# Kernel tuning notes

Hardware: AMD Instinct MI355X
Metric: run time of the kernel (lower is better)

## Reference

```python
import jax, jax.numpy as jnp
import numpy as np
from jax.scipy.linalg import expm

B, Q, F, R, T, H = 2048, 16, 512, 400, 50, 256
STEPS = 100
DT = 1.0 / STEPS
COH = 50.0  # coherence_time


def setup_inputs() -> dict:
    ks = jax.random.split(jax.random.key(0), 48)
    it = iter(range(48))
    def rn(shape, s=1.0):
        return jax.random.normal(ks[next(it)], shape, dtype=jnp.float32) * s
    A = rn((Q, Q)); Bm = rn((Q, Q))
    d = {
        'molecular_features': rn((B, F)),
        'noise': rn((B, T, R), 0.1),          # torch.randn_like * 0.1
        'amp_re': rn((B, Q)), 'amp_im': rn((B, Q)),
        'H_re': (A + A.T) / 2.0,               # hermitized: real part symmetric
        'H_im': (Bm - Bm.T) / 2.0,             # imag part antisymmetric
        'gpc': rn((R,)),
        'bw1': rn((256, Q + F), (Q + F) ** -0.5), 'bb1': rn((256,), 0.01),
        'bw2': rn((128, 256), 256 ** -0.5), 'bb2': rn((128,), 0.01),
        'bw3': rn((R, 128), 128 ** -0.5), 'bb3': rn((R,), 0.01),
    }
    ins = [R, H, H]
    for l in range(3):
        d[f'Wih{l}'] = rn((4 * H, ins[l]), ins[l] ** -0.5)
        d[f'Whh{l}'] = rn((4 * H, H), H ** -0.5)
        d[f'bih{l}'] = rn((4 * H,), 0.01)
        d[f'bhh{l}'] = rn((4 * H,), 0.01)
    d.update({
        'cw1': rn((512, H + R), (H + R) ** -0.5), 'cb1': rn((512,), 0.01),
        'cw2': rn((256, 512), 512 ** -0.5), 'cb2': rn((256,), 0.01),
        'cw3': rn((64, 256), 256 ** -0.5), 'cb3': rn((64,), 0.01),
        'cw4': rn((1, 64), 64 ** -0.5), 'cb4': rn((1,), 0.01),
    })
    return d


def _lstm_layer(x, Wih, Whh, bih, bhh):
    # PyTorch LSTM gate order: i, f, g, o
    def step(carry, xt):
        h, c = carry
        z = xt @ Wih.T + h @ Whh.T + bih + bhh
        ig, fg, gg, og = jnp.split(z, 4, axis=-1)
        c = jax.nn.sigmoid(fg) * c + jax.nn.sigmoid(ig) * jnp.tanh(gg)
        h = jax.nn.sigmoid(og) * jnp.tanh(c)
        return (h, c), h
    n = x.shape[0]
    init = (jnp.zeros((n, H), x.dtype), jnp.zeros((n, H), x.dtype))
    (hT, _), hs = jax.lax.scan(step, init, jnp.swapaxes(x, 0, 1))
    return jnp.swapaxes(hs, 0, 1), hT


def _forward(molecular_features, noise, amp_re, amp_im, H_re, H_im, gpc,
             bw1, bb1, bw2, bb2, bw3, bb3,
             Wih0, Whh0, bih0, bhh0, Wih1, Whh1, bih1, bhh1, Wih2, Whh2, bih2, bhh2,
             cw1, cb1, cw2, cb2, cw3, cb3, cw4, cb4):
    Hp = (H_re + 1j * H_im).astype(jnp.complex64)
    amp = (amp_re + 1j * amp_im).astype(jnp.complex64)
    amp = amp / jnp.linalg.norm(amp, axis=-1, keepdims=True)  # F.normalize
    # molecular interaction Hamiltonian (real part only, as in source)
    M = jnp.einsum('bi,ij->bij', molecular_features[:, :Q], H_re)
    def qstep(a, step):
        t = step * DT
        Ht = Hp[None, :, :] + M * t                 # [B,Q,Q] complex
        U = jax.vmap(expm)(-1j * Ht * DT)           # per-sample matrix_exp
        a = jnp.einsum('bij,bj->bi', U, a) * jnp.exp(-t / COH)
        return a, None
    amp, _ = jax.lax.scan(qstep, amp, jnp.arange(STEPS, dtype=jnp.float32))
    obs = (jnp.abs(amp) ** 2).astype(jnp.float32)   # quantum observables
    bio = jnp.concatenate([obs, molecular_features], axis=-1)  # [B, Q+F]
    h1 = jax.nn.relu(bio @ bw1.T + bb1)
    h2 = jnp.tanh(h1 @ bw2.T + bb2)
    receptor = jax.nn.sigmoid(h2 @ bw3.T + bb3)     # [B, R]
    # biological signal transduction
    g_amp = receptor * jax.nn.sigmoid(gpc)
    adapt = jnp.exp(-jnp.arange(T, dtype=jnp.float32) / 10.0)[None, :, None]
    seq = g_amp[:, None, :] * adapt + noise         # [B, T, R]
    x, hT = _lstm_layer(seq, Wih0, Whh0, bih0, bhh0)
    x, hT = _lstm_layer(x, Wih1, Whh1, bih1, bhh1)
    x, hT = _lstm_layer(x, Wih2, Whh2, bih2, bhh2)  # hT: last-layer hidden [B,H]
    cf = jnp.concatenate([hT, receptor], axis=-1)   # [B, H+R]
    c1 = jax.nn.relu(cf @ cw1.T + cb1)
    c2 = jax.nn.relu(c1 @ cw2.T + cb2)
    c3 = jnp.tanh(c2 @ cw3.T + cb3)
    cons = jnp.mean(jax.nn.sigmoid(c3 @ cw4.T + cb4))
    valence = jnp.mean(jnp.tanh(x), axis=(1, 2))    # [B]
    return receptor, x, valence, cons, amp


def reference(molecular_features, noise, amp_re, amp_im, H_re, H_im, gpc,
              bw1, bb1, bw2, bb2, bw3, bb3,
              Wih0, Whh0, bih0, bhh0, Wih1, Whh1, bih1, bhh1, Wih2, Whh2, bih2, bhh2,
              cw1, cb1, cw2, cb2, cw3, cb3, cw4, cb4):
    receptor, seq, valence, cons, amp = _forward(
        molecular_features, noise, amp_re, amp_im, H_re, H_im, gpc,
        bw1, bb1, bw2, bb2, bw3, bb3,
        Wih0, Whh0, bih0, bhh0, Wih1, Whh1, bih1, bhh1, Wih2, Whh2, bih2, bhh2,
        cw1, cb1, cw2, cb2, cw3, cb3, cw4, cb4)
    # von Neumann entanglement entropy across a 2/2 qubit bipartition (Q=16 -> 4x4)
    half = 2 ** ((int(np.log2(Q))) // 2)
    rs = amp.reshape(amp.shape[0], half, -1)
    rho = jnp.einsum('bij,bik->bjk', rs, jnp.conj(rs))
    ev = jnp.clip(jnp.linalg.eigvals(rho).real, 1e-12, None)
    ent = jnp.mean(-jnp.sum(ev * jnp.log(ev), axis=-1))
    return receptor, seq, valence, cons, ent
```

## Files before the change

### kernel.cpp

```cpp
#include <hip/hip_runtime.h>
#include <stdint.h>


using short8 = __attribute__((ext_vector_type(8))) short;
using f32x4  = __attribute__((ext_vector_type(4))) float;

#define DEV static __device__ __forceinline__

typedef const __attribute__((address_space(1))) void GV;
typedef __attribute__((address_space(3))) void LV;
DEV void gload16(const void* g, void* l) {
  __builtin_amdgcn_global_load_lds((GV*)g, (LV*)l, 16, 0, 0);
}

DEV ushort f2b(float x) {
  union { float f; uint32_t u; } v; v.f = x;
  uint32_t r = v.u + 0x7FFFu + ((v.u >> 16) & 1u);
  return (ushort)(r >> 16);
}
DEV float b2f(ushort x) {
  union { uint32_t u; float f; } v; v.u = ((uint32_t)x) << 16; return v.f;
}
DEV float sigf(float x) { return 1.f / (1.f + __expf(-x)); }
DEV float tanh_fast(float x) {
  float xc = fminf(9.f, fmaxf(-9.f, x));
  float e = __expf(2.f * xc);
  return (e - 1.f) / (e + 1.f);
}

__global__ void k_convw(const float* __restrict__ src, ushort* __restrict__ dst,
                        int sr, int dr, int sc, int dc,
                        const float* __restrict__ scale, int mode) {
  long n = (long)dr * dc;
  for (long idx = (long)blockIdx.x * blockDim.x + threadIdx.x; idx < n;
       idx += (long)gridDim.x * blockDim.x) {
    int r = (int)(idx / dc), c = (int)(idx % dc);
    float v = 0.f;
    if (r < sr && c < sc) {
      v = src[(long)r * sc + c];
      if (mode == 1) v *= sigf(scale[c]);
    }
    dst[idx] = f2b(v);
  }
}

__global__ void k_vadd(const float* __restrict__ a, const float* __restrict__ b,
                       float* __restrict__ o, int n) {
  int i = blockIdx.x * blockDim.x + threadIdx.x;
  if (i < n) o[i] = a[i] + b[i];
}

__global__ __launch_bounds__(128)
void k_quantum(const float* __restrict__ ampr_in, const float* __restrict__ ampi_in,
               const float* __restrict__ Hre, const float* __restrict__ Him,
               const float* __restrict__ mf,
               ushort* __restrict__ bio, float* __restrict__ ampS_r,
               float* __restrict__ ampS_i, int st0) {
  const int gid = blockIdx.x * 128 + threadIdx.x;
  const int b = gid >> 5;
  const int l32 = gid & 31;
  const int i = l32 & 15;
  const int h = l32 >> 4;
  float hre[8], him[8];
#pragma unroll
  for (int jj = 0; jj < 8; jj++) {
    hre[jj] = Hre[i * 16 + h * 8 + jj];
    him[jj] = Him[i * 16 + h * 8 + jj];
  }
  const float mfi = mf[(long)b * 512 + i];
  float are, aim;
  if (st0 == 0) {
    are = ampr_in[b * 16 + i]; aim = ampi_in[b * 16 + i];
    float ss = are * are + aim * aim;
#pragma unroll
    for (int m = 1; m < 32; m <<= 1) ss += __shfl_xor(ss, m, 32);
    ss *= 0.5f;
    const float inv = 1.f / sqrtf(ss);
    are *= inv; aim *= inv;
  } else {
    are = ampS_r[b * 16 + i]; aim = ampS_i[b * 16 + i];
  }
#pragma unroll 1
  for (int st = st0; st < st0 + 25; ++st) {
    const float t = (float)st * 0.01f;
    const float fac = 1.f + t * mfi;
    const float dec = __expf(-t * 0.02f);
    float tre = are, tim = aim, rre = are, rim = aim;
#pragma unroll 1
    for (int k = 1; k <= 5; k++) {
      float w1r = 0.f, w1i = 0.f, w2r = 0.f, w2i = 0.f;
#pragma unroll
      for (int jj = 0; jj < 8; jj++) {
        const float vr = __shfl(tre, h * 8 + jj, 32);
        const float vi = __shfl(tim, h * 8 + jj, 32);
        w1r += hre[jj] * vr; w1i += hre[jj] * vi;
        w2r += him[jj] * vr; w2i += him[jj] * vi;
      }
      w1r += __shfl_xor(w1r, 16, 32);
      w1i += __shfl_xor(w1i, 16, 32);
      w2r += __shfl_xor(w2r, 16, 32);
      w2i += __shfl_xor(w2i, 16, 32);
      const float hr = w1r * fac - w2i;
      const float hi = w1i * fac + w2r;
      const float sk = 0.01f / (float)k;
      tre = sk * hi; tim = -sk * hr;
      rre += tre; rim += tim;
    }
    are = rre * dec; aim = rim * dec;
  }
  if (h == 0) {
    ampS_r[b * 16 + i] = are;
    ampS_i[b * 16 + i] = aim;
    if (bio) bio[(long)b * 576 + i] = f2b(are * are + aim * aim);
  }
}

__global__ void k_biofill(const float* __restrict__ mf, ushort* __restrict__ bio) {
  long i = (long)blockIdx.x * blockDim.x + threadIdx.x;
  if (i < (long)2048 * 512) {
    long b = i >> 9, k = i & 511;
    bio[b * 576 + 16 + k] = f2b(mf[i]);
  }
}

template<int BT>
__global__ __launch_bounds__(256)
void k_gemm(const ushort* __restrict__ A, int lda,
            const ushort* __restrict__ W, int ldw,
            const float* __restrict__ bias,
            const ushort* __restrict__ Gg, int t0,
            float* __restrict__ Cf, int ldcf,
            ushort* __restrict__ Cb, int ldcb,
            int N, int K, int act, int swz) {
  constexpr int FR = BT / 32;
  constexpr int CH = BT / 32;
  __shared__ __align__(16) ushort lsA[2][BT * 64];
  __shared__ __align__(16) ushort lsB[2][BT * 64];
  const int tid = threadIdx.x;
  const int lane = tid & 63, w = tid >> 6;
  const int lr = lane & 15, lq = lane >> 4;
  const int wm = (w >> 1) * (BT / 2), wn = (w & 1) * (BT / 2);
  int bxb = blockIdx.x, byb = blockIdx.y;
  if (swz) {
    const int id = byb * gridDim.x + bxb;
    const int xcd = id & 7, q = id >> 3;
    byb = (q >> 4) * 16 + xcd * 2 + (q & 1);
    bxb = (q >> 1) & 7;
  }
  const int bm = byb * BT, bn = bxb * BT;
  const int srow = lane >> 3;
  const int scol = (((lane & 7) ^ srow)) * 8;

  auto stage = [&](int buf, int kk) {
#pragma unroll
    for (int c = 0; c < CH; c++) {
      const int ch = w * CH + c;
      const int r = ch * 8 + srow;
      gload16(A + (size_t)(bm + r) * lda + kk + scol, lsA[buf] + ch * 512);
      gload16(W + (size_t)(bn + r) * ldw + kk + scol, lsB[buf] + ch * 512);
    }
  };

  f32x4 acc[FR][FR];
#pragma unroll
  for (int i = 0; i < FR; i++)
#pragma unroll
    for (int j = 0; j < FR; j++) acc[i][j] = (f32x4){0.f, 0.f, 0.f, 0.f};

  stage(0, 0);
  __syncthreads();
  const int T = K >> 6;
  for (int t = 0; t < T; t++) {
    const int cur = t & 1;
    if (t + 1 < T) stage(cur ^ 1, (t + 1) * 64);
    short8 af[FR][2], bf[FR][2];
#pragma unroll
    for (int mi = 0; mi < FR; mi++)
#pragma unroll
      for (int k2 = 0; k2 < 2; k2++) {
        const int row = wm + mi * 16 + lr;
        af[mi][k2] = *(const short8*)(lsA[cur] + (row >> 3) * 512 + (row & 7) * 64 +
                                      (((k2 * 4 + lq) ^ (row & 7)) * 8));
      }
#pragma unroll
    for (int ni = 0; ni < FR; ni++)
#pragma unroll
      for (int k2 = 0; k2 < 2; k2++) {
        const int row = wn + ni * 16 + lr;
        bf[ni][k2] = *(const short8*)(lsB[cur] + (row >> 3) * 512 + (row & 7) * 64 +
                                      (((k2 * 4 + lq) ^ (row & 7)) * 8));
      }
#pragma unroll
    for (int k2 = 0; k2 < 2; k2++)
#pragma unroll
      for (int mi = 0; mi < FR; mi++)
#pragma unroll
        for (int ni = 0; ni < FR; ni++)
          acc[mi][ni] = __builtin_amdgcn_mfma_f32_16x16x32_bf16(
              af[mi][k2], bf[ni][k2], acc[mi][ni], 0, 0, 0);
    __syncthreads();
  }

#pragma unroll
  for (int mi = 0; mi < FR; mi++) {
#pragma unroll
    for (int r = 0; r < 4; r++) {
      const int row = bm + wm + mi * 16 + lq * 4 + r;
      float gfac = 0.f; const ushort* ggrow = nullptr;
      if (Gg) {
        gfac = __expf(-(float)(t0 + (row >> 11)) * 0.1f);
        ggrow = Gg + (size_t)(row & 2047) * 1024;
      }
#pragma unroll
      for (int ni = 0; ni < FR; ni++) {
        const int col = bn + wn + ni * 16 + lr;
        if (col < N) {
          float v = acc[mi][ni][r];
          if (bias) v += bias[col];
          if (Gg)  v += gfac * b2f(ggrow[col]);
          if (act == 1) v = fmaxf(v, 0.f);
          else if (act == 2) v = tanh_fast(v);
          else if (act == 3) v = sigf(v);
          if (Cf) Cf[(size_t)row * ldcf + col] = v;
          if (Cb) Cb[(size_t)row * ldcb + col] = f2b(v);
        }
      }
    }
  }
}

__global__ void k_noiseconv(const float* __restrict__ noise, ushort* __restrict__ dst, int t0) {
  long n = 10L * 2048 * 448;
  for (long idx = (long)blockIdx.x * blockDim.x + threadIdx.x; idx < n;
       idx += (long)gridDim.x * blockDim.x) {
    int r = (int)(idx % 448);
    long row = idx / 448;
    int b = (int)(row & 2047);
    int tl = (int)(row >> 11);
    ushort v = 0;
    if (r < 400)
      v = f2b(__builtin_nontemporal_load(&noise[((long)b * 50 + t0 + tl) * 400 + r]));
    dst[idx] = v;
  }
}

__global__ __launch_bounds__(512, 2)
void k_fused(const ushort* __restrict__ IH, const ushort* __restrict__ Whh,
             float* __restrict__ hstate, float* __restrict__ cstate,
             ushort* __restrict__ Hout, float* __restrict__ Xout, int t0,
             const ushort* __restrict__ gA, int glda,
             const ushort* __restrict__ gW,
             const float* __restrict__ gbias, const ushort* __restrict__ gGg,
             int gt0, ushort* __restrict__ gC, int gK) {
  __shared__ __align__(16) ushort upool[37024];
  const int tid = threadIdx.x;

  if (blockIdx.x < 128) {
    ushort (*h_lds)[266] = (ushort(*)[266])upool;
    ushort* ih0 = upool + 4256;
    const int lane = tid & 63, w8 = tid >> 6;
    const int lr = lane & 15, lq = lane >> 4;
    const int b0 = blockIdx.x * 16;
    const int wcols = w8 * 32;

    short8 wres[2][8];
#pragma unroll
    for (int cg = 0; cg < 2; cg++) {
      const ushort* wp = Whh + (size_t)(wcols + cg * 16 + lr) * 256 + lq * 8;
#pragma unroll
      for (int kk = 0; kk < 8; kk++) wres[cg][kk] = *(const short8*)(wp + kk * 32);
    }

    float c_reg[2][4], h_reg[2][4];
#pragma unroll
    for (int cg = 0; cg < 2; cg++) {
      const int j = wcols + cg * 16 + lr;
#pragma unroll
      for (int r = 0; r < 4; r++) {
        const int s = lq * 4 + r;
        float hv = hstate[(size_t)(b0 + s) * 256 + j];
        c_reg[cg][r] = cstate[(size_t)(b0 + s) * 256 + j];
        h_reg[cg][r] = hv;
        h_lds[s][j] = f2b(hv);
      }
    }
    __syncthreads();

#define LOADB(buf, g, cg) { \
  const ushort* wp_ = Whh + (size_t)((g) * 256 + wcols + (cg) * 16 + lr) * 256 + lq * 8; \
  _Pragma("unroll") for (int kk = 0; kk < 8; kk++) (buf)[kk] = *(const short8*)(wp_ + kk * 32); }
#define MFMAB(buf, g, cg) { \
  _Pragma("unroll") for (int kk = 0; kk < 8; kk++) \
    acc[cg][g] = __builtin_amdgcn_mfma_f32_16x16x32_bf16(af[kk], (buf)[kk], acc[cg][g], 0, 0, 0); }
#define MFMAR(cg) { \
  _Pragma("unroll") for (int kk = 0; kk < 8; kk++) \
    acc[cg][0] = __builtin_amdgcn_mfma_f32_16x16x32_bf16(af[kk], wres[cg][kk], acc[cg][0], 0, 0, 0); }

    for (int blk = 0; blk < 10; blk += 2) {
#pragma unroll
      for (int si = 0; si < 2; si++) {
        const ushort* src = IH + ((size_t)(blk + si) * 2048 + b0) * 1024;
#pragma unroll
        for (int u = 0; u < 4; u++) {
          const int bi = u * 8 + w8;
          gload16(src + (size_t)bi * 512 + lane * 8, ih0 + si * 16384 + bi * 512);
        }
      }
      __syncthreads();

      for (int i2 = 0; i2 < 2; i2++) {
        const int tl = blk + i2;
        const ushort* ihc = ih0 + i2 * 16384;
        short8 af[8];
#pragma unroll
        for (int kk = 0; kk < 8; kk++)
          af[kk] = *(const short8*)(&h_lds[lr][kk * 32 + lq * 8]);
        __syncthreads();

        f32x4 acc[2][4];
#pragma unroll
        for (int cg = 0; cg < 2; cg++)
#pragma unroll
          for (int g = 0; g < 4; g++) acc[cg][g] = (f32x4){0.f, 0.f, 0.f, 0.f};

        short8 wb0[8], wb1[8];
        LOADB(wb0, 1, 0);
        LOADB(wb1, 1, 1);
        MFMAR(0);
        MFMAR(1);
        MFMAB(wb0, 1, 0);
        LOADB(wb0, 2, 0);
        MFMAB(wb1, 1, 1);
        LOADB(wb1, 2, 1);
        MFMAB(wb0, 2, 0);
        LOADB(wb0, 3, 0);
        MFMAB(wb1, 2, 1);
        LOADB(wb1, 3, 1);
        MFMAB(wb0, 3, 0);
        MFMAB(wb1, 3, 1);

        const int t = t0 + tl;
#pragma unroll
        for (int cg = 0; cg < 2; cg++) {
          const int j = wcols + cg * 16 + lr;
#pragma unroll
          for (int r = 0; r < 4; r++) {
            const int s = lq * 4 + r;
            const float zi = acc[cg][0][r] + b2f(ihc[s * 1024 + j]);
            const float zf = acc[cg][1][r] + b2f(ihc[s * 1024 + 256 + j]);
            const float zg = acc[cg][2][r] + b2f(ihc[s * 1024 + 512 + j]);
            const float zo = acc[cg][3][r] + b2f(ihc[s * 1024 + 768 + j]);
            const float ig = sigf(zi), fg = sigf(zf), gg = tanh_fast(zg), og = sigf(zo);
            const float c = fg * c_reg[cg][r] + ig * gg;
            c_reg[cg][r] = c;
            const float h = og * tanh_fast(c);
            h_reg[cg][r] = h;
            h_lds[s][j] = f2b(h);
            if (Hout) Hout[((size_t)t * 2048 + b0 + s) * 256 + j] = f2b(h);
            if (Xout)
              __builtin_nontemporal_store(h, &Xout[((size_t)(b0 + s) * 50 + t) * 256 + j]);
          }
        }
        __syncthreads();
      }
    }
#undef LOADB
#undef MFMAB
#undef MFMAR
#pragma unroll
    for (int cg = 0; cg < 2; cg++) {
      const int j = wcols + cg * 16 + lr;
#pragma unroll
      for (int r = 0; r < 4; r++) {
        const int s = lq * 4 + r;
        hstate[(size_t)(b0 + s) * 256 + j] = h_reg[cg][r];
        cstate[(size_t)(b0 + s) * 256 + j] = c_reg[cg][r];
      }
    }
  } else {
    ushort* lsA = upool;
    ushort* lsB = upool + 16384;
    const int gb = blockIdx.x - 128;
    const int xcd = gb & 7, q = gb >> 3;
    const int byb = (q >> 4) * 16 + xcd * 2 + (q & 1);
    const int bxb = (q >> 1) & 7;
    const int bm = byb * 128, bn = bxb * 128;
    const int lane = tid & 63, wg = tid >> 6;
    const int lr = lane & 15, lq = lane >> 4;
    const int wm = (wg >> 2) * 64, wn = (wg & 3) * 32;
    const int srow = lane >> 3;
    const int scol = (((lane & 7) ^ srow)) * 8;

    f32x4 acc[4][2];
#pragma unroll
    for (int i = 0; i < 4; i++)
#pragma unroll
      for (int j = 0; j < 2; j++) acc[i][j] = (f32x4){0.f, 0.f, 0.f, 0.f};

#pragma unroll
    for (int c = 0; c < 2; c++) {
      const int ch = wg * 2 + c;
      const int r = ch * 8 + srow;
      gload16(gA + (size_t)(bm + r) * glda + scol, lsA + ch * 512);
      gload16(gW + (size_t)(bn + r) * glda + scol, lsB + ch * 512);
    }
    __syncthreads();

    const int T = gK >> 6;
    for (int t = 0; t < T; t++) {
      const int cur = t & 1;
      if (t + 1 < T) {
        const int kk = (t + 1) * 64;
#pragma unroll
        for (int c = 0; c < 2; c++) {
          const int ch = wg * 2 + c;
          const int r = ch * 8 + srow;
          gload16(gA + (size_t)(bm + r) * glda + kk + scol, lsA + (cur ^ 1) * 8192 + ch * 512);
          gload16(gW + (size_t)(bn + r) * glda + kk + scol, lsB + (cur ^ 1) * 8192 + ch * 512);
        }
      }
      {
        short8 af[4][2], bf[2][2];
#pragma unroll
        for (int mi = 0; mi < 4; mi++)
#pragma unroll
          for (int k2 = 0; k2 < 2; k2++) {
            const int row = wm + mi * 16 + lr;
            af[mi][k2] = *(const short8*)(lsA + cur * 8192 + (row >> 3) * 512 +
                                          (row & 7) * 64 + (((k2 * 4 + lq) ^ (row & 7)) * 8));
          }
#pragma unroll
        for (int ni = 0; ni < 2; ni++)
#pragma unroll
          for (int k2 = 0; k2 < 2; k2++) {
            const int row = wn + ni * 16 + lr;
            bf[ni][k2] = *(const short8*)(lsB + cur * 8192 + (row >> 3) * 512 +
                                          (row & 7) * 64 + (((k2 * 4 + lq) ^ (row & 7)) * 8));
          }
#pragma unroll
        for (int k2 = 0; k2 < 2; k2++)
#pragma unroll
          for (int mi = 0; mi < 4; mi++)
#pragma unroll
            for (int ni = 0; ni < 2; ni++)
              acc[mi][ni] = __builtin_amdgcn_mfma_f32_16x16x32_bf16(
                  af[mi][k2], bf[ni][k2], acc[mi][ni], 0, 0, 0);
      }
      __syncthreads();
    }

    {
#pragma unroll
      for (int mi = 0; mi < 4; mi++) {
#pragma unroll
        for (int r = 0; r < 4; r++) {
          const int row = bm + wm + mi * 16 + lq * 4 + r;
          float gfac = 0.f; const ushort* ggrow = nullptr;
          if (gGg) {
            gfac = __expf(-(float)(gt0 + (row >> 11)) * 0.1f);
            ggrow = gGg + (size_t)(row & 2047) * 1024;
          }
#pragma unroll
          for (int ni = 0; ni < 2; ni++) {
            const int col = bn + wn + ni * 16 + lr;
            float v = acc[mi][ni][r];
            if (gbias) v += gbias[col];
            if (gGg)  v += gfac * b2f(ggrow[col]);
            gC[(size_t)row * 1024 + col] = f2b(v);
          }
        }
      }
    }
  }
}

__global__ void k_cffill(const float* __restrict__ hT, const ushort* __restrict__ recb,
                         ushort* __restrict__ cf) {
  long i = (long)blockIdx.x * blockDim.x + threadIdx.x;
  if (i < (long)2048 * 656) {
    long b = i / 656; int c = (int)(i % 656);
    cf[b * 704 + c] = (c < 256) ? f2b(hT[b * 256 + c]) : recb[b * 448 + (c - 256)];
  }
}

__global__ __launch_bounds__(256)
void k_cons(const float* __restrict__ c3, const float* __restrict__ w4,
            const float* __restrict__ b4, float* __restrict__ out) {
  __shared__ float red[256];
  float accv = 0.f;
  for (int b = threadIdx.x; b < 2048; b += 256) {
    float d = b4[0];
#pragma unroll
    for (int k = 0; k < 64; k++) d += c3[(long)b * 64 + k] * w4[k];
    accv += sigf(d);
  }
  red[threadIdx.x] = accv; __syncthreads();
  for (int s = 128; s > 0; s >>= 1) {
    if (threadIdx.x < s) red[threadIdx.x] += red[threadIdx.x + s];
    __syncthreads();
  }
  if (threadIdx.x == 0) out[0] = red[0] * (1.f / 2048.f);
}

__global__ __launch_bounds__(256)
void k_val(const float* __restrict__ x, float* __restrict__ out) {
  __shared__ float red[256];
  const float* p = x + (size_t)blockIdx.x * 12800;
  float a = 0.f;
  for (int i = threadIdx.x; i < 12800; i += 256) a += tanh_fast(p[i]);
  red[threadIdx.x] = a; __syncthreads();
  for (int s = 128; s > 0; s >>= 1) {
    if (threadIdx.x < s) red[threadIdx.x] += red[threadIdx.x + s];
    __syncthreads();
  }
  if (threadIdx.x == 0) out[blockIdx.x] = red[0] * (1.f / 12800.f);
}

__global__ __launch_bounds__(64)
void k_ent(const float* __restrict__ ar, const float* __restrict__ ai,
           float* __restrict__ partial) {
  __shared__ float red[64];
  const int tid = threadIdx.x;
  const int b = blockIdx.x * 64 + tid;
  float vr[16], vi[16];
#pragma unroll
  for (int i = 0; i < 16; i++) { vr[i] = ar[b * 16 + i]; vi[i] = ai[b * 16 + i]; }
  float m[64];
#pragma unroll
  for (int j = 0; j < 4; j++)
#pragma unroll
    for (int k = 0; k < 4; k++) {
      float re = 0.f, im = 0.f;
#pragma unroll
      for (int i = 0; i < 4; i++) {
        float xr = vr[i * 4 + j], xi = vi[i * 4 + j];
        float yr = vr[i * 4 + k], yi = vi[i * 4 + k];
        re += xr * yr + xi * yi;
        im += xi * yr - xr * yi;
      }
      m[j * 8 + k] = re;
      m[j * 8 + (k + 4)] = -im;
      m[(j + 4) * 8 + k] = im;
      m[(j + 4) * 8 + (k + 4)] = re;
    }
#pragma unroll 1
  for (int sweep = 0; sweep < 6; ++sweep) {
#pragma unroll
    for (int p = 0; p < 7; p++) {
#pragma unroll
      for (int q = p + 1; q < 8; q++) {
        const float apq = m[p * 8 + q];
        if (fabsf(apq) > 1e-28f) {
          const float app = m[p * 8 + p], aqq = m[q * 8 + q];
          const float tau = (aqq - app) / (2.f * apq);
          const float tt = (tau >= 0.f ? 1.f : -1.f) /
                           (fabsf(tau) + sqrtf(1.f + tau * tau));
          const float cc = 1.f / sqrtf(1.f + tt * tt);
          const float ssn = tt * cc;
#pragma unroll
          for (int k2 = 0; k2 < 8; k2++) {
            const float mp = m[p * 8 + k2], mq = m[q * 8 + k2];
            m[p * 8 + k2] = cc * mp - ssn * mq;
            m[q * 8 + k2] = ssn * mp + cc * mq;
          }
#pragma unroll
          for (int k2 = 0; k2 < 8; k2++) {
            const float mp = m[k2 * 8 + p], mq = m[k2 * 8 + q];
            m[k2 * 8 + p] = cc * mp - ssn * mq;
            m[k2 * 8 + q] = ssn * mp + cc * mq;
          }
        }
      }
    }
  }
  float e = 0.f;
#pragma unroll
  for (int k2 = 0; k2 < 8; k2++) {
    const float lam = fmaxf(m[k2 * 8 + k2], 1e-12f);
    e -= lam * logf(lam);
  }
  red[tid] = e; __syncthreads();
  for (int s = 32; s > 0; s >>= 1) {
    if (tid < s) red[tid] += red[tid + s];
    __syncthreads();
  }
  if (tid == 0) partial[blockIdx.x] = red[0];
}

__global__ void k_entfin(const float* __restrict__ partial, float* __restrict__ out) {
  if (threadIdx.x == 0) {
    float s = 0.f;
    for (int i = 0; i < 32; i++) s += partial[i];
    out[0] = s * (0.5f / 2048.f);
  }
}

extern "C" void kernel_launch(void* const* d_in, const int* in_sizes, int n_in,
                              void* d_out, int out_size, void* d_ws, size_t ws_size,
                              hipStream_t stream) {
  (void)in_sizes; (void)n_in; (void)out_size; (void)ws_size;
  const float* mf    = (const float*)d_in[0];
  const float* noise = (const float*)d_in[1];
  const float* ampr  = (const float*)d_in[2];
  const float* ampi  = (const float*)d_in[3];
  const float* Hre   = (const float*)d_in[4];
  const float* Him   = (const float*)d_in[5];
  const float* gpc   = (const float*)d_in[6];
  const float* bw1 = (const float*)d_in[7];  const float* bb1 = (const float*)d_in[8];
  const float* bw2 = (const float*)d_in[9];  const float* bb2 = (const float*)d_in[10];
  const float* bw3 = (const float*)d_in[11]; const float* bb3 = (const float*)d_in[12];
  const float* Wih[3] = {(const float*)d_in[13], (const float*)d_in[17], (const float*)d_in[21]};
  const float* Whh[3] = {(const float*)d_in[14], (const float*)d_in[18], (const float*)d_in[22]};
  const float* bih[3] = {(const float*)d_in[15], (const float*)d_in[19], (const float*)d_in[23]};
  const float* bhh[3] = {(const float*)d_in[16], (const float*)d_in[20], (const float*)d_in[24]};
  const float* cw1 = (const float*)d_in[25]; const float* cb1 = (const float*)d_in[26];
  const float* cw2 = (const float*)d_in[27]; const float* cb2 = (const float*)d_in[28];
  const float* cw3 = (const float*)d_in[29]; const float* cb3 = (const float*)d_in[30];
  const float* cw4 = (const float*)d_in[31]; const float* cb4 = (const float*)d_in[32];

  float* out = (float*)d_out;
  float* out_rec  = out;
  float* out_seq  = out + 819200;
  float* out_val  = out + 27033600;
  float* out_cons = out + 27035648;
  float* out_ent  = out + 27035649;

  char* ws = (char*)d_ws;
  size_t off = 0;
  auto alloc = [&](size_t bytes) -> char* {
    char* p = ws + off; off += (bytes + 255) & ~(size_t)255; return p;
  };
  ushort* WB1   = (ushort*)alloc((size_t)256 * 576 * 2);
  ushort* WB2   = (ushort*)alloc((size_t)128 * 256 * 2);
  ushort* WB3   = (ushort*)alloc((size_t)512 * 128 * 2);
  ushort* WIH0  = (ushort*)alloc((size_t)1024 * 448 * 2);
  ushort* WIH0S = (ushort*)alloc((size_t)1024 * 448 * 2);
  ushort* WIH1  = (ushort*)alloc((size_t)1024 * 256 * 2);
  ushort* WIH2  = (ushort*)alloc((size_t)1024 * 256 * 2);
  ushort* WHH0  = (ushort*)alloc((size_t)1024 * 256 * 2);
  ushort* WHH1  = (ushort*)alloc((size_t)1024 * 256 * 2);
  ushort* WHH2  = (ushort*)alloc((size_t)1024 * 256 * 2);
  ushort* WC1   = (ushort*)alloc((size_t)512 * 704 * 2);
  ushort* WC2   = (ushort*)alloc((size_t)256 * 512 * 2);
  ushort* WC3   = (ushort*)alloc((size_t)128 * 256 * 2);
  float*  BSUM  = (float*)alloc((size_t)3 * 1024 * 4);
  ushort* BIO   = (ushort*)alloc((size_t)2048 * 576 * 2);
  ushort* H1B   = (ushort*)alloc((size_t)2048 * 256 * 2);
  ushort* H2B   = (ushort*)alloc((size_t)2048 * 128 * 2);
  ushort* RECB  = (ushort*)alloc((size_t)2048 * 448 * 2);
  ushort* GGB   = (ushort*)alloc((size_t)2048 * 1024 * 2);
  float*  AMPR  = (float*)alloc((size_t)2048 * 16 * 4);
  float*  AMPI  = (float*)alloc((size_t)2048 * 16 * 4);
  ushort* NCH   = (ushort*)alloc((size_t)10 * 2048 * 448 * 2);
  ushort* IHCA  = (ushort*)alloc((size_t)10 * 2048 * 1024 * 2);
  ushort* IHCB  = (ushort*)alloc((size_t)10 * 2048 * 1024 * 2);
  ushort* HBUF  = (ushort*)alloc((size_t)50 * 2048 * 256 * 2);
  float*  HST   = (float*)alloc((size_t)2048 * 256 * 4);
  float*  CST   = (float*)alloc((size_t)2048 * 256 * 4);
  ushort* CFB   = (ushort*)alloc((size_t)2048 * 704 * 2);
  ushort* C1B   = (ushort*)alloc((size_t)2048 * 512 * 2);
  ushort* C2B   = (ushort*)alloc((size_t)2048 * 256 * 2);
  float*  C3F   = (float*)alloc((size_t)2048 * 64 * 4);
  float*  ENTP  = (float*)alloc((size_t)32 * 4);

  hipMemsetAsync(BIO,  0, (size_t)2048 * 576 * 2, stream);
  hipMemsetAsync(RECB, 0, (size_t)2048 * 448 * 2, stream);
  hipMemsetAsync(CFB,  0, (size_t)2048 * 704 * 2, stream);

  auto convw = [&](const float* src, ushort* dst, int sr, int dr, int sc, int dc,
                   const float* scale, int mode) {
    long n = (long)dr * dc;
    int blocks = (int)((n + 255) / 256); if (blocks > 2048) blocks = 2048;
    hipLaunchKernelGGL(k_convw, dim3(blocks), dim3(256), 0, stream,
                       src, dst, sr, dr, sc, dc, scale, mode);
  };
  convw(bw1, WB1, 256, 256, 528, 576, nullptr, 0);
  convw(bw2, WB2, 128, 128, 256, 256, nullptr, 0);
  convw(bw3, WB3, 400, 512, 128, 128, nullptr, 0);
  convw(Wih[0], WIH0,  1024, 1024, 400, 448, nullptr, 0);
  convw(Wih[0], WIH0S, 1024, 1024, 400, 448, gpc, 1);
  convw(Wih[1], WIH1, 1024, 1024, 256, 256, nullptr, 0);
  convw(Wih[2], WIH2, 1024, 1024, 256, 256, nullptr, 0);
  convw(Whh[0], WHH0, 1024, 1024, 256, 256, nullptr, 0);
  convw(Whh[1], WHH1, 1024, 1024, 256, 256, nullptr, 0);
  convw(Whh[2], WHH2, 1024, 1024, 256, 256, nullptr, 0);
  convw(cw1, WC1, 512, 512, 656, 704, nullptr, 0);
  convw(cw2, WC2, 256, 256, 512, 512, nullptr, 0);
  convw(cw3, WC3,  64, 128, 256, 256, nullptr, 0);
  for (int l = 0; l < 3; l++)
    hipLaunchKernelGGL(k_vadd, dim3(4), dim3(256), 0, stream, bih[l], bhh[l], BSUM + l * 1024, 1024);

  for (int qc = 0; qc < 4; qc++)
    hipLaunchKernelGGL(k_quantum, dim3(512), dim3(128), 0, stream,
                       ampr, ampi, Hre, Him, mf,
                       (qc == 3 ? BIO : (ushort*)nullptr), AMPR, AMPI, qc * 25);
  hipLaunchKernelGGL(k_biofill, dim3(4096), dim3(256), 0, stream, mf, BIO);

  auto gemm = [&](bool big, const ushort* A, int lda, const ushort* W, int ldw,
                  const float* bias, const ushort* Gg, int t0, float* Cf, int ldcf,
                  ushort* Cb, int ldcb, int M, int N, int K, int act) {
    if (big) {
      dim3 grid((N + 127) / 128, M / 128);
      const int swz = (grid.x == 8 && (grid.y & 15) == 0) ? 1 : 0;
      hipLaunchKernelGGL(k_gemm<128>, grid, dim3(256), 0, stream,
                         A, lda, W, ldw, bias, Gg, t0, Cf, ldcf, Cb, ldcb, N, K, act, swz);
    } else {
      dim3 grid((N + 63) / 64, M / 64);
      hipLaunchKernelGGL(k_gemm<64>, grid, dim3(256), 0, stream,
                         A, lda, W, ldw, bias, Gg, t0, Cf, ldcf, Cb, ldcb, N, K, act, 0);
    }
  };

  gemm(false, BIO, 576, WB1, 576, bb1, nullptr, 0, nullptr, 0, H1B, 256, 2048, 256, 576, 1);
  gemm(false, H1B, 256, WB2, 256, bb2, nullptr, 0, nullptr, 0, H2B, 128, 2048, 128, 256, 2);
  gemm(false, H2B, 128, WB3, 128, bb3, nullptr, 0, out_rec, 400, RECB, 448, 2048, 400, 128, 3);
  gemm(false, RECB, 448, WIH0S, 448, nullptr, nullptr, 0, nullptr, 0, GGB, 1024, 2048, 1024, 448, 0);

  const ushort* WHHl[3] = {WHH0, WHH1, WHH2};
  ushort* IHCbuf[2] = {IHCA, IHCB};
  hipLaunchKernelGGL(k_noiseconv, dim3(8192), dim3(256), 0, stream, noise, NCH, 0);
  gemm(true, NCH, 448, WIH0, 448, BSUM, GGB, 0, nullptr, 0, IHCA, 1024, 20480, 1024, 448, 0);

  for (int i = 0; i < 15; i++) {
    const int l = i / 5, c = i % 5;
    if (c == 0) hipMemsetAsync(HST, 0, (size_t)2048 * 256 * 4 * 2, stream);
    const bool hg = (i + 1 < 15);
    const ushort* gA = nullptr; const ushort* gWp = nullptr;
    const float* gb_ = nullptr; const ushort* gGg = nullptr;
    int glda = 256, gK = 256, ggt0 = 0;
    if (hg) {
      const int l2 = (i + 1) / 5, c2 = (i + 1) % 5;
      if (l2 == 0) {
        hipLaunchKernelGGL(k_noiseconv, dim3(8192), dim3(256), 0, stream, noise, NCH, c2 * 10);
        gA = NCH; glda = 448; gK = 448; gb_ = BSUM; gGg = GGB; ggt0 = c2 * 10; gWp = WIH0;
      } else {
        gA = HBUF + (size_t)(c2 * 10) * 2048 * 256; glda = 256; gK = 256;
        gb_ = BSUM + l2 * 1024; gGg = nullptr; ggt0 = 0;
        gWp = (l2 == 1 ? WIH1 : WIH2);
      }
    }
    dim3 grid(hg ? 1408 : 128);
    hipLaunchKernelGGL(k_fused, grid, dim3(512), 0, stream,
                       IHCbuf[i & 1], WHHl[l], HST, CST,
                       (l < 2 ? HBUF : (ushort*)nullptr),
                       (l == 2 ? out_seq : (float*)nullptr), c * 10,
                       gA, glda, gWp, gb_, gGg, ggt0, IHCbuf[(i + 1) & 1], gK);
  }

  hipLaunchKernelGGL(k_cffill, dim3(5256), dim3(256), 0, stream, HST, RECB, CFB);
  gemm(false, CFB, 704, WC1, 704, cb1, nullptr, 0, nullptr, 0, C1B, 512, 2048, 512, 704, 1);
  gemm(false, C1B, 512, WC2, 512, cb2, nullptr, 0, nullptr, 0, C2B, 256, 2048, 256, 512, 1);
  gemm(false, C2B, 256, WC3, 256, cb3, nullptr, 0, C3F, 64, nullptr, 0, 2048, 64, 256, 2);
  hipLaunchKernelGGL(k_cons, dim3(1), dim3(256), 0, stream, C3F, cw4, cb4, out_cons);

  hipLaunchKernelGGL(k_val, dim3(2048), dim3(256), 0, stream, out_seq, out_val);
  hipLaunchKernelGGL(k_ent, dim3(32), dim3(64), 0, stream, AMPR, AMPI, ENTP);
  hipLaunchKernelGGL(k_entfin, dim3(1), dim3(32), 0, stream, ENTP, out_ent);
}
```

Baseline: 2.644 ms.

## Merge quantum evolution into one launch and add 512-thread GEMM for first input projection

```diff
diff --git a/kernel.cpp b/kernel.cpp
--- a/kernel.cpp
+++ b/kernel.cpp
@@ -54,8 +54,8 @@
 void k_quantum(const float* __restrict__ ampr_in, const float* __restrict__ ampi_in,
                const float* __restrict__ Hre, const float* __restrict__ Him,
                const float* __restrict__ mf,
-               ushort* __restrict__ bio, float* __restrict__ ampS_r,
-               float* __restrict__ ampS_i, int st0) {
+               ushort* __restrict__ bio, float* __restrict__ ampr_out,
+               float* __restrict__ ampi_out) {
   const int gid = blockIdx.x * 128 + threadIdx.x;
   const int b = gid >> 5;
   const int l32 = gid & 31;
@@ -68,20 +68,15 @@
     him[jj] = Him[i * 16 + h * 8 + jj];
   }
   const float mfi = mf[(long)b * 512 + i];
-  float are, aim;
-  if (st0 == 0) {
-    are = ampr_in[b * 16 + i]; aim = ampi_in[b * 16 + i];
-    float ss = are * are + aim * aim;
-#pragma unroll
-    for (int m = 1; m < 32; m <<= 1) ss += __shfl_xor(ss, m, 32);
-    ss *= 0.5f;
-    const float inv = 1.f / sqrtf(ss);
-    are *= inv; aim *= inv;
-  } else {
-    are = ampS_r[b * 16 + i]; aim = ampS_i[b * 16 + i];
-  }
+  float are = ampr_in[b * 16 + i], aim = ampi_in[b * 16 + i];
+  float ss = are * are + aim * aim;
+#pragma unroll
+  for (int m = 1; m < 32; m <<= 1) ss += __shfl_xor(ss, m, 32);
+  ss *= 0.5f;
+  const float inv = 1.f / sqrtf(ss);
+  are *= inv; aim *= inv;
 #pragma unroll 1
-  for (int st = st0; st < st0 + 25; ++st) {
+  for (int st = 0; st < 100; ++st) {
     const float t = (float)st * 0.01f;
     const float fac = 1.f + t * mfi;
     const float dec = __expf(-t * 0.02f);
@@ -109,9 +104,9 @@
     are = rre * dec; aim = rim * dec;
   }
   if (h == 0) {
-    ampS_r[b * 16 + i] = are;
-    ampS_i[b * 16 + i] = aim;
-    if (bio) bio[(long)b * 576 + i] = f2b(are * are + aim * aim);
+    ampr_out[b * 16 + i] = are;
+    ampi_out[b * 16 + i] = aim;
+    bio[(long)b * 576 + i] = f2b(are * are + aim * aim);
   }
 }
 
@@ -224,6 +219,105 @@
           if (Cf) Cf[(size_t)row * ldcf + col] = v;
           if (Cb) Cb[(size_t)row * ldcb + col] = f2b(v);
         }
+      }
+    }
+  }
+}
+
+__global__ __launch_bounds__(512, 2)
+void k_gemm8(const ushort* __restrict__ gA, int glda,
+             const ushort* __restrict__ gW,
+             const float* __restrict__ gbias, const ushort* __restrict__ gGg,
+             int gt0, ushort* __restrict__ gC, int gK) {
+  __shared__ __align__(16) ushort lsA[2 * 8192];
+  __shared__ __align__(16) ushort lsB[2 * 8192];
+  const int tid = threadIdx.x;
+  const int gb = blockIdx.x;
+  const int xcd = gb & 7, q = gb >> 3;
+  const int byb = (q >> 4) * 16 + xcd * 2 + (q & 1);
+  const int bxb = (q >> 1) & 7;
+  const int bm = byb * 128, bn = bxb * 128;
+  const int lane = tid & 63, wg = tid >> 6;
+  const int lr = lane & 15, lq = lane >> 4;
+  const int wm = (wg >> 2) * 64, wn = (wg & 3) * 32;
+  const int srow = lane >> 3;
+  const int scol = (((lane & 7) ^ srow)) * 8;
+
+  f32x4 acc[4][2];
+#pragma unroll
+  for (int i = 0; i < 4; i++)
+#pragma unroll
+    for (int j = 0; j < 2; j++) acc[i][j] = (f32x4){0.f, 0.f, 0.f, 0.f};
+
+#pragma unroll
+  for (int c = 0; c < 2; c++) {
+    const int ch = wg * 2 + c;
+    const int r = ch * 8 + srow;
+    gload16(gA + (size_t)(bm + r) * glda + scol, lsA + ch * 512);
+    gload16(gW + (size_t)(bn + r) * glda + scol, lsB + ch * 512);
+  }
+  __syncthreads();
+
+  const int T = gK >> 6;
+  for (int t = 0; t < T; t++) {
+    const int cur = t & 1;
+    if (t + 1 < T) {
+      const int kk = (t + 1) * 64;
+#pragma unroll
+      for (int c = 0; c < 2; c++) {
+        const int ch = wg * 2 + c;
+        const int r = ch * 8 + srow;
+        gload16(gA + (size_t)(bm + r) * glda + kk + scol, lsA + (cur ^ 1) * 8192 + ch * 512);
+        gload16(gW + (size_t)(bn + r) * glda + kk + scol, lsB + (cur ^ 1) * 8192 + ch * 512);
+      }
+    }
+    {
+      short8 af[4][2], bf[2][2];
+#pragma unroll
+      for (int mi = 0; mi < 4; mi++)
+#pragma unroll
+        for (int k2 = 0; k2 < 2; k2++) {
+          const int row = wm + mi * 16 + lr;
+          af[mi][k2] = *(const short8*)(lsA + cur * 8192 + (row >> 3) * 512 +
+                                        (row & 7) * 64 + (((k2 * 4 + lq) ^ (row & 7)) * 8));
+        }
+#pragma unroll
+      for (int ni = 0; ni < 2; ni++)
+#pragma unroll
+        for (int k2 = 0; k2 < 2; k2++) {
+          const int row = wn + ni * 16 + lr;
+          bf[ni][k2] = *(const short8*)(lsB + cur * 8192 + (row >> 3) * 512 +
+                                        (row & 7) * 64 + (((k2 * 4 + lq) ^ (row & 7)) * 8));
+        }
+#pragma unroll
+      for (int k2 = 0; k2 < 2; k2++)
+#pragma unroll
+        for (int mi = 0; mi < 4; mi++)
+#pragma unroll
+          for (int ni = 0; ni < 2; ni++)
+            acc[mi][ni] = __builtin_amdgcn_mfma_f32_16x16x32_bf16(
+                af[mi][k2], bf[ni][k2], acc[mi][ni], 0, 0, 0);
+    }
+    __syncthreads();
+  }
+
+#pragma unroll
+  for (int mi = 0; mi < 4; mi++) {
+#pragma unroll
+    for (int r = 0; r < 4; r++) {
+      const int row = bm + wm + mi * 16 + lq * 4 + r;
+      float gfac = 0.f; const ushort* ggrow = nullptr;
+      if (gGg) {
+        gfac = __expf(-(float)(gt0 + (row >> 11)) * 0.1f);
+        ggrow = gGg + (size_t)(row & 2047) * 1024;
+      }
+#pragma unroll
+      for (int ni = 0; ni < 2; ni++) {
+        const int col = bn + wn + ni * 16 + lr;
+        float v = acc[mi][ni][r];
+        if (gbias) v += gbias[col];
+        if (gGg)  v += gfac * b2f(ggrow[col]);
+        gC[(size_t)row * 1024 + col] = f2b(v);
       }
     }
   }
@@ -690,10 +784,8 @@
   for (int l = 0; l < 3; l++)
     hipLaunchKernelGGL(k_vadd, dim3(4), dim3(256), 0, stream, bih[l], bhh[l], BSUM + l * 1024, 1024);
 
-  for (int qc = 0; qc < 4; qc++)
-    hipLaunchKernelGGL(k_quantum, dim3(512), dim3(128), 0, stream,
-                       ampr, ampi, Hre, Him, mf,
-                       (qc == 3 ? BIO : (ushort*)nullptr), AMPR, AMPI, qc * 25);
+  hipLaunchKernelGGL(k_quantum, dim3(512), dim3(128), 0, stream,
+                     ampr, ampi, Hre, Him, mf, BIO, AMPR, AMPI);
   hipLaunchKernelGGL(k_biofill, dim3(4096), dim3(256), 0, stream, mf, BIO);
 
   auto gemm = [&](bool big, const ushort* A, int lda, const ushort* W, int ldw,
@@ -719,7 +811,8 @@
   const ushort* WHHl[3] = {WHH0, WHH1, WHH2};
   ushort* IHCbuf[2] = {IHCA, IHCB};
   hipLaunchKernelGGL(k_noiseconv, dim3(8192), dim3(256), 0, stream, noise, NCH, 0);
-  gemm(true, NCH, 448, WIH0, 448, BSUM, GGB, 0, nullptr, 0, IHCA, 1024, 20480, 1024, 448, 0);
+  hipLaunchKernelGGL(k_gemm8, dim3(1280), dim3(512), 0, stream,
+                     NCH, 448, WIH0, BSUM, GGB, 0, IHCA, 448);
 
   for (int i = 0; i < 15; i++) {
     const int l = i / 5, c = i % 5;
```

After: 2.598 ms. No clear change (-1.7%).
